# Kernel tuning notes

Hardware: AMD Instinct MI355X
Metric: run time of the kernel (lower is better)

The kernel has to match this reference:

```python
import jax, jax.numpy as jnp
import numpy as np

IN_FEAT = 3 * 299 * 299  # 268203
D1 = 512
H = 28
OUT = 2


def setup_inputs() -> dict:
    key = jax.random.key(0)
    ks = jax.random.split(key, 10)
    B, T = 4, 64
    s1 = 1.0 / np.sqrt(IN_FEAT)
    s2 = 1.0 / np.sqrt(D1)
    s3 = 1.0 / np.sqrt(H)
    return {
        "x": jax.random.normal(ks[0], (B, T, 3, 299, 299), jnp.float32),
        "W1": jax.random.uniform(ks[1], (IN_FEAT, D1), jnp.float32, -s1, s1),
        "b1": jax.random.uniform(ks[2], (D1,), jnp.float32, -s1, s1),
        "Wi": jax.random.uniform(ks[3], (D1, H), jnp.float32, -s2, s2),
        "Wr": jax.random.uniform(ks[4], (H, H), jnp.float32, -s3, s3),
        "br": jax.random.uniform(ks[5], (H,), jnp.float32, -s3, s3),
        "A": jax.random.normal(ks[6], (H,), jnp.float32),
        "tau": 1.0 + jax.random.uniform(ks[7], (H,), jnp.float32),  # positive time constants
        "W2": jax.random.uniform(ks[8], (H, OUT), jnp.float32, -s3, s3),
        "b2": jax.random.uniform(ks[9], (OUT,), jnp.float32, -s3, s3),
    }


def reference(x, W1, b1, Wi, Wr, br, A, tau, W2, b2):
    B, T = x.shape[0], x.shape[1]
    xf = x.reshape(B, T, -1)                      # [B, T, 268203]
    h1 = jax.nn.relu(jnp.einsum('btf,fd->btd', xf, W1) + b1)  # [B, T, 512]
    u = jnp.einsum('btd,dh->bth', h1, Wi)         # precomputed input drive [B, T, H]
    dt = 1.0

    def step(h, u_t):
        # fused-Euler LTC cell: f gates both time-constant and attractor A
        ft = jax.nn.sigmoid(u_t + h @ Wr + br)
        h_new = (h + dt * ft * A) / (1.0 + dt * (1.0 / tau + ft))
        return h_new, h_new

    h0 = jnp.zeros((B, H), x.dtype)
    _, hs = jax.lax.scan(step, h0, jnp.swapaxes(u, 0, 1))  # [T, B, H]
    last = jax.nn.relu(hs[-1])                    # relu then take last step
    out = last @ W2 + b2                          # [B, 2]
    return jax.nn.sigmoid(out)
```

## Files before the change

### kernel.cpp

```cpp
#include <hip/hip_runtime.h>
#include <hip/hip_bf16.h>

#define KTOT   268203
#define MROWS  256
#define NCOLS  512
#define HDIM   28
#define NSTEPS 8382
#define FSTEP  8381
#define KREM   11
#define BN     256
#define BROWS  40

typedef __attribute__((ext_vector_type(4))) float        f32x4;
typedef __attribute__((ext_vector_type(4))) unsigned int u32x4;
typedef __attribute__((ext_vector_type(8))) __bf16       bf16x8;

static __device__ inline bf16x8 pack8(const float* f) {
    union { bf16x8 v; __hip_bfloat16 h[8]; } u;
    #pragma unroll
    for (int j = 0; j < 8; ++j) u.h[j] = __float2bfloat16(f[j]);
    return u.v;
}
static __device__ inline unsigned short bfbits(float v) {
    __hip_bfloat16 h = __float2bfloat16(v);
    union { __hip_bfloat16 h; unsigned short u; } c; c.h = h; return c.u;
}

__global__ __launch_bounds__(512, 2) void gemm1_kernel(
    const float* __restrict__ x, const float* __restrict__ W1,
    __hip_bfloat16* __restrict__ part, int steps_per, int nks)
{
    __shared__ __align__(16) float          Albuf[2][MROWS * 32];
    __shared__ __align__(16) __hip_bfloat16 Blds[2][BN * BROWS];

    const int tid  = threadIdx.x;
    const int lane = tid & 63;
    const int w    = tid >> 6;
    const int wm   = w >> 1;
    const int wn   = w & 1;

    int bx, ks;
    {
        const int id = blockIdx.x;
        if ((nks & 7) == 0) {
            const int xcd = id & 7;
            const int m_  = id >> 3;
            bx = m_ & 1;
            ks = ((m_ >> 1) << 3) | xcd;
        } else {
            bx = id & 1;
            ks = id >> 1;
        }
    }
    const int bcol = bx * BN;

    const int dlt = lane >> 5;
    const int m   = lane & 31;
    const int rw7 = (2 * w + dlt) & 7;
    const int ag  = (m >> 2) ^ rw7;
    const size_t a_off = (size_t)(2 * w + dlt) * KTOT + ag * 4 + (m & 3);
    const int bkh  = w >> 2;
    const int bcl  = (w & 3) * 64 + lane;

    f32x4 acc[4][8];
    #pragma unroll
    for (int i = 0; i < 4; ++i)
        #pragma unroll
        for (int j = 0; j < 8; ++j)
            acc[i][j] = (f32x4){0.f, 0.f, 0.f, 0.f};

    const int s0 = ks * steps_per;
    int s1 = s0 + steps_per;
    if (s1 > NSTEPS) s1 = NSTEPS;
    int s1f = (s1 < FSTEP) ? s1 : FSTEP;
    int nfull = s1f - s0;
    if (nfull < 0) nfull = 0;

    float bregA[16], bregB[16];

    auto issueA = [&](int s, int buf) {
        const float* ap = x + a_off + (size_t)s * 32;
        #pragma unroll
        for (int i = 0; i < 16; ++i) {
            const float* gp = ap + (size_t)i * 16 * KTOT;
            char* lp = (char*)&Albuf[buf][0] + (i * 8 + w) * 256;
            __builtin_amdgcn_global_load_lds(
                (const __attribute__((address_space(1))) unsigned int*)(const void*)gp,
                (__attribute__((address_space(3))) unsigned int*)(void*)lp, 4, 0, 0);
        }
    };
    auto loadB = [&](int s, float* breg) {
        const float* bp = W1 + ((size_t)s * 32 + bkh * 16) * NCOLS + bcol + bcl;
        #pragma unroll
        for (int kk = 0; kk < 16; ++kk)
            breg[kk] = bp[(size_t)kk * NCOLS];
    };
    auto writeB = [&](const float* breg, int buf) {
        unsigned int pk[8];
        #pragma unroll
        for (int q = 0; q < 8; ++q)
            pk[q] = (unsigned int)bfbits(breg[2 * q]) |
                    ((unsigned int)bfbits(breg[2 * q + 1]) << 16);
        __hip_bfloat16* dst = &Blds[buf][bcl * BROWS + bkh * 16];
        *(u32x4*)(dst)     = (u32x4){pk[0], pk[1], pk[2], pk[3]};
        *(u32x4*)(dst + 8) = (u32x4){pk[4], pk[5], pk[6], pk[7]};
    };

    auto compute = [&](int buf) {
        const int rc = lane & 15, ko = lane >> 4;
        bf16x8 bq[8];
        #pragma unroll
        for (int ni = 0; ni < 8; ++ni)
            bq[ni] = *(const bf16x8*)&Blds[buf][(wn * 128 + ni * 16 + rc) * BROWS + ko * 8];
        const int soff = ((2 * ko) ^ (rc & 7)) * 16;
        #pragma unroll
        for (int mi = 0; mi < 4; ++mi) {
            const int ab = (wm * 64 + mi * 16 + rc) * 128;
            float afv[8];
            *(f32x4*)&afv[0] = *(const f32x4*)((const char*)&Albuf[buf][0] + ab + soff);
            *(f32x4*)&afv[4] = *(const f32x4*)((const char*)&Albuf[buf][0] + ab + (soff ^ 16));
            const bf16x8 af = pack8(afv);
            #pragma unroll
            for (int ni = 0; ni < 8; ++ni)
                acc[mi][ni] = __builtin_amdgcn_mfma_f32_16x16x32_bf16(
                    af, bq[ni], acc[mi][ni], 0, 0, 0);
        }
    };

    if (nfull > 0) {
        issueA(s0, 0); loadB(s0, bregA);
        if (nfull > 1) { issueA(s0 + 1, 1); loadB(s0 + 1, bregB); }
        int t = 0;
        for (;;) {
            if (t + 1 < nfull) { asm volatile("s_waitcnt vmcnt(32)" ::: "memory"); }
            else               { asm volatile("s_waitcnt vmcnt(0)"  ::: "memory"); }
            __builtin_amdgcn_sched_barrier(0);
            writeB(bregA, 0);
            asm volatile("s_waitcnt lgkmcnt(0)" ::: "memory");
            __builtin_amdgcn_sched_barrier(0);
            __builtin_amdgcn_s_barrier();
            __builtin_amdgcn_sched_barrier(0);
            compute(0);
            __builtin_amdgcn_sched_barrier(0);
            __builtin_amdgcn_s_barrier();
            if (t + 2 < nfull) { issueA(s0 + t + 2, 0); loadB(s0 + t + 2, bregA); }
            if (++t >= nfull) break;
            if (t + 1 < nfull) { asm volatile("s_waitcnt vmcnt(32)" ::: "memory"); }
            else               { asm volatile("s_waitcnt vmcnt(0)"  ::: "memory"); }
            __builtin_amdgcn_sched_barrier(0);
            writeB(bregB, 1);
            asm volatile("s_waitcnt lgkmcnt(0)" ::: "memory");
            __builtin_amdgcn_sched_barrier(0);
            __builtin_amdgcn_s_barrier();
            __builtin_amdgcn_sched_barrier(0);
            compute(1);
            __builtin_amdgcn_sched_barrier(0);
            __builtin_amdgcn_s_barrier();
            if (t + 2 < nfull) { issueA(s0 + t + 2, 1); loadB(s0 + t + 2, bregB); }
            if (++t >= nfull) break;
        }
    }

    if (s1 > FSTEP && s0 < s1) {
        const int buf = nfull & 1;
        __syncthreads();
        {
            const int row = tid >> 1, half = tid & 1;
            #pragma unroll
            for (int i = 0; i < 16; ++i) {
                const int k = half * 16 + i;
                const float v = (k < KREM)
                    ? x[(size_t)row * KTOT + (size_t)FSTEP * 32 + k] : 0.f;
                Albuf[buf][row * 32 + ((k >> 2) ^ (row & 7)) * 4 + (k & 3)] = v;
            }
        }
        {
            const int c = tid & 255, og = tid >> 8;
            #pragma unroll
            for (int i = 0; i < 16; ++i) {
                const int k = og * 16 + i;
                const float v = (k < KREM)
                    ? W1[(size_t)(FSTEP * 32 + k) * NCOLS + bcol + c] : 0.f;
                Blds[buf][c * BROWS + k] = __float2bfloat16(v);
            }
        }
        __syncthreads();
        compute(buf);
    }

    __hip_bfloat16* outp = part + (size_t)ks * MROWS * NCOLS;
    const int rc = lane & 15, q = lane >> 4;
    #pragma unroll
    for (int mi = 0; mi < 4; ++mi) {
        #pragma unroll
        for (int ni = 0; ni < 8; ++ni) {
            const int col = bcol + wn * 128 + ni * 16 + rc;
            #pragma unroll
            for (int j = 0; j < 4; ++j) {
                const int row = wm * 64 + mi * 16 + q * 4 + j;
                const float v  = acc[mi][ni][j];
                const float vh = __shfl_xor(v, 1);
                if (!(rc & 1)) {
                    const unsigned int pk =
                        (unsigned int)bfbits(v) | ((unsigned int)bfbits(vh) << 16);
                    *(unsigned int*)(outp + (size_t)row * NCOLS + col) = pk;
                }
            }
        }
    }
}

__global__ __launch_bounds__(512) void reduce_u_kernel(
    const __hip_bfloat16* __restrict__ part, const float* __restrict__ b1,
    const float* __restrict__ Wi, float* __restrict__ u, int nks)
{
    __shared__ float h1[NCOLS];
    __shared__ f32x4 red[4][128];
    const int row = blockIdx.x;
    const int tid = threadIdx.x;
    const int c4  = tid & 127;
    const int kk  = tid >> 7;

    const unsigned short* pu = (const unsigned short*)part;
    f32x4 sum = (f32x4){0.f, 0.f, 0.f, 0.f};
    for (int k = kk; k < nks; k += 4) {
        const size_t base = ((size_t)k * MROWS + row) * NCOLS + c4 * 4;
        ushort4 pv = *(const ushort4*)&pu[base];
        union { unsigned int u; float f; } c0, c1, c2, c3;
        c0.u = (unsigned int)pv.x << 16; c1.u = (unsigned int)pv.y << 16;
        c2.u = (unsigned int)pv.z << 16; c3.u = (unsigned int)pv.w << 16;
        sum[0] += c0.f; sum[1] += c1.f; sum[2] += c2.f; sum[3] += c3.f;
    }
    red[kk][c4] = sum;
    __syncthreads();

    if (tid < 128) {
        f32x4 t = red[0][tid] + red[1][tid] + red[2][tid] + red[3][tid];
        const f32x4 bb = *(const f32x4*)&b1[tid * 4];
        t += bb;
        #pragma unroll
        for (int j = 0; j < 4; ++j) h1[tid * 4 + j] = fmaxf(t[j], 0.f);
    }
    __syncthreads();

    const int wv = tid >> 6, lane = tid & 63;
    #pragma unroll
    for (int hh = 0; hh < 4; ++hh) {
        const int h = wv * 4 + hh;
        if (h < HDIM) {
            float p = 0.f;
            #pragma unroll
            for (int dd = 0; dd < 8; ++dd) {
                const int d = lane + dd * 64;
                p += h1[d] * Wi[d * HDIM + h];
            }
            #pragma unroll
            for (int off = 32; off; off >>= 1) p += __shfl_down(p, off);
            if (lane == 0) u[row * HDIM + h] = p;
        }
    }
}

__global__ __launch_bounds__(64) void recur_kernel(
    const float* __restrict__ u, const float* __restrict__ Wr,
    const float* __restrict__ br, const float* __restrict__ Av,
    const float* __restrict__ tau, const float* __restrict__ W2,
    const float* __restrict__ b2, float* __restrict__ out)
{
    const int b = blockIdx.x;
    const int j = threadIdx.x;
    const bool act = j < HDIM;
    const int jj = act ? j : 0;

    float wr[HDIM];
    #pragma unroll
    for (int i = 0; i < HDIM; ++i) wr[i] = act ? Wr[i * HDIM + jj] : 0.f;
    const float brj = act ? br[jj] : 0.f;
    const float Aj  = act ? Av[jj] : 0.f;
    const float itj = act ? (1.f / tau[jj]) : 0.f;

    float uv[64];
    #pragma unroll
    for (int t = 0; t < 64; ++t)
        uv[t] = act ? u[(b * 64 + t) * HDIM + jj] : 0.f;

    float h = 0.f;
    #pragma unroll
    for (int t = 0; t < 64; ++t) {
        float a = uv[t] + brj;
        #pragma unroll
        for (int i = 0; i < HDIM; ++i)
            a += __shfl(h, i) * wr[i];
        const float ft = 1.f / (1.f + expf(-a));
        const float hn = (h + ft * Aj) / (1.f + itj + ft);
        h = act ? hn : 0.f;
    }

    const float r  = act ? fmaxf(h, 0.f) : 0.f;
    float p0 = act ? r * W2[jj * 2 + 0] : 0.f;
    float p1 = act ? r * W2[jj * 2 + 1] : 0.f;
    #pragma unroll
    for (int off = 32; off; off >>= 1) {
        p0 += __shfl_down(p0, off);
        p1 += __shfl_down(p1, off);
    }
    if (j == 0) {
        out[b * 2 + 0] = 1.f / (1.f + expf(-(p0 + b2[0])));
        out[b * 2 + 1] = 1.f / (1.f + expf(-(p1 + b2[1])));
    }
}

extern "C" void kernel_launch(void* const* d_in, const int* in_sizes, int n_in,
                              void* d_out, int out_size, void* d_ws, size_t ws_size,
                              hipStream_t stream)
{
    (void)in_sizes; (void)n_in; (void)out_size;
    const float* x   = (const float*)d_in[0];
    const float* W1  = (const float*)d_in[1];
    const float* b1  = (const float*)d_in[2];
    const float* Wi  = (const float*)d_in[3];
    const float* Wr  = (const float*)d_in[4];
    const float* br  = (const float*)d_in[5];
    const float* Av  = (const float*)d_in[6];
    const float* tau = (const float*)d_in[7];
    const float* W2  = (const float*)d_in[8];
    const float* b2  = (const float*)d_in[9];
    float* out = (float*)d_out;

    const size_t per_split = (size_t)MROWS * NCOLS * sizeof(__hip_bfloat16);
    int nks = 128;
    while (nks > 8 && (size_t)nks * per_split + (1 << 16) > ws_size) nks >>= 1;
    const int steps_per = (NSTEPS + nks - 1) / nks;

    __hip_bfloat16* part = (__hip_bfloat16*)d_ws;
    float* u = (float*)((char*)d_ws + (size_t)nks * per_split);

    gemm1_kernel<<<dim3(2 * nks), 512, 0, stream>>>(x, W1, part, steps_per, nks);
    reduce_u_kernel<<<dim3(MROWS), 512, 0, stream>>>(part, b1, Wi, u, nks);
    recur_kernel<<<dim3(4), 64, 0, stream>>>(u, Wr, br, Av, tau, W2, b2, out);
}
```

Before: 270.3 us.

## Shrink GEMM1 column tile to 128 with 256-thread blocks and 4x grid

Halves the N tile of the split-K GEMM from 256 to 128 columns and the block from 8 to 4 waves, launching four column blocks per K-split instead of two. Each wave now covers 64 rows by all 128 columns, the B LDS tile drops its padding (stride 32 instead of 40), and each thread issues 32 direct-to-LDS A loads per step instead of 16. The aim is more blocks and smaller LDS per block for better occupancy and latency hiding. The cost is that the x tile, the dominant operand, is now read from global memory four times instead of twice, and the unpadded B layout may cause LDS bank conflicts.

```diff
diff --git a/kernel.cpp b/kernel.cpp
--- a/kernel.cpp
+++ b/kernel.cpp
@@ -8,8 +8,7 @@
 #define NSTEPS 8382
 #define FSTEP  8381
 #define KREM   11
-#define BN     256
-#define BROWS  40
+#define BN     128
 
 typedef __attribute__((ext_vector_type(4))) float        f32x4;
 typedef __attribute__((ext_vector_type(4))) unsigned int u32x4;
@@ -26,41 +25,40 @@
     union { __hip_bfloat16 h; unsigned short u; } c; c.h = h; return c.u;
 }
 
-__global__ __launch_bounds__(512, 2) void gemm1_kernel(
+__global__ __launch_bounds__(256, 2) void gemm1_kernel(
     const float* __restrict__ x, const float* __restrict__ W1,
     __hip_bfloat16* __restrict__ part, int steps_per, int nks)
 {
     __shared__ __align__(16) float          Albuf[2][MROWS * 32];
-    __shared__ __align__(16) __hip_bfloat16 Blds[2][BN * BROWS];
+    __shared__ __align__(16) __hip_bfloat16 Blds[2][BN * 32];
 
     const int tid  = threadIdx.x;
     const int lane = tid & 63;
     const int w    = tid >> 6;
-    const int wm   = w >> 1;
-    const int wn   = w & 1;
+    const int wm   = w;
 
     int bx, ks;
     {
         const int id = blockIdx.x;
         if ((nks & 7) == 0) {
-            const int xcd = id & 7;
-            const int m_  = id >> 3;
-            bx = m_ & 1;
-            ks = ((m_ >> 1) << 3) | xcd;
+            const int xcd  = id & 7;
+            const int rest = id >> 3;
+            bx = rest & 3;
+            ks = ((rest >> 2) << 3) | xcd;
         } else {
-            bx = id & 1;
-            ks = id >> 1;
+            bx = id & 3;
+            ks = id >> 2;
         }
     }
     const int bcol = bx * BN;
 
     const int dlt = lane >> 5;
     const int m   = lane & 31;
-    const int rw7 = (2 * w + dlt) & 7;
+    const int rw7 = 2 * w + dlt;
     const int ag  = (m >> 2) ^ rw7;
-    const size_t a_off = (size_t)(2 * w + dlt) * KTOT + ag * 4 + (m & 3);
-    const int bkh  = w >> 2;
-    const int bcl  = (w & 3) * 64 + lane;
+    const size_t a_off = (size_t)rw7 * KTOT + ag * 4 + (m & 3);
+    const int bcl = tid & 127;
+    const int bkh = tid >> 7;
 
     f32x4 acc[4][8];
     #pragma unroll
@@ -81,9 +79,9 @@
     auto issueA = [&](int s, int buf) {
         const float* ap = x + a_off + (size_t)s * 32;
         #pragma unroll
-        for (int i = 0; i < 16; ++i) {
-            const float* gp = ap + (size_t)i * 16 * KTOT;
-            char* lp = (char*)&Albuf[buf][0] + (i * 8 + w) * 256;
+        for (int i = 0; i < 32; ++i) {
+            const float* gp = ap + (size_t)i * 8 * KTOT;
+            char* lp = (char*)&Albuf[buf][0] + (i * 8 + 2 * w) * 128;
             __builtin_amdgcn_global_load_lds(
                 (const __attribute__((address_space(1))) unsigned int*)(const void*)gp,
                 (__attribute__((address_space(3))) unsigned int*)(void*)lp, 4, 0, 0);
@@ -101,7 +99,7 @@
         for (int q = 0; q < 8; ++q)
             pk[q] = (unsigned int)bfbits(breg[2 * q]) |
                     ((unsigned int)bfbits(breg[2 * q + 1]) << 16);
-        __hip_bfloat16* dst = &Blds[buf][bcl * BROWS + bkh * 16];
+        __hip_bfloat16* dst = &Blds[buf][bcl * 32 + bkh * 16];
         *(u32x4*)(dst)     = (u32x4){pk[0], pk[1], pk[2], pk[3]};
         *(u32x4*)(dst + 8) = (u32x4){pk[4], pk[5], pk[6], pk[7]};
     };
@@ -111,7 +109,7 @@
         bf16x8 bq[8];
         #pragma unroll
         for (int ni = 0; ni < 8; ++ni)
-            bq[ni] = *(const bf16x8*)&Blds[buf][(wn * 128 + ni * 16 + rc) * BROWS + ko * 8];
+            bq[ni] = *(const bf16x8*)&Blds[buf][(ni * 16 + rc) * 32 + ko * 8];
         const int soff = ((2 * ko) ^ (rc & 7)) * 16;
         #pragma unroll
         for (int mi = 0; mi < 4; ++mi) {
@@ -132,7 +130,7 @@
         if (nfull > 1) { issueA(s0 + 1, 1); loadB(s0 + 1, bregB); }
         int t = 0;
         for (;;) {
-            if (t + 1 < nfull) { asm volatile("s_waitcnt vmcnt(32)" ::: "memory"); }
+            if (t + 1 < nfull) { asm volatile("s_waitcnt vmcnt(48)" ::: "memory"); }
             else               { asm volatile("s_waitcnt vmcnt(0)"  ::: "memory"); }
             __builtin_amdgcn_sched_barrier(0);
             writeB(bregA, 0);
@@ -145,7 +143,7 @@
             __builtin_amdgcn_s_barrier();
             if (t + 2 < nfull) { issueA(s0 + t + 2, 0); loadB(s0 + t + 2, bregA); }
             if (++t >= nfull) break;
-            if (t + 1 < nfull) { asm volatile("s_waitcnt vmcnt(32)" ::: "memory"); }
+            if (t + 1 < nfull) { asm volatile("s_waitcnt vmcnt(48)" ::: "memory"); }
             else               { asm volatile("s_waitcnt vmcnt(0)"  ::: "memory"); }
             __builtin_amdgcn_sched_barrier(0);
             writeB(bregB, 1);
@@ -165,23 +163,21 @@
         const int buf = nfull & 1;
         __syncthreads();
         {
-            const int row = tid >> 1, half = tid & 1;
-            #pragma unroll
-            for (int i = 0; i < 16; ++i) {
-                const int k = half * 16 + i;
+            const int row = tid;
+            #pragma unroll
+            for (int k = 0; k < 32; ++k) {
                 const float v = (k < KREM)
                     ? x[(size_t)row * KTOT + (size_t)FSTEP * 32 + k] : 0.f;
                 Albuf[buf][row * 32 + ((k >> 2) ^ (row & 7)) * 4 + (k & 3)] = v;
             }
         }
         {
-            const int c = tid & 255, og = tid >> 8;
             #pragma unroll
             for (int i = 0; i < 16; ++i) {
-                const int k = og * 16 + i;
+                const int k = bkh * 16 + i;
                 const float v = (k < KREM)
-                    ? W1[(size_t)(FSTEP * 32 + k) * NCOLS + bcol + c] : 0.f;
-                Blds[buf][c * BROWS + k] = __float2bfloat16(v);
+                    ? W1[(size_t)(FSTEP * 32 + k) * NCOLS + bcol + bcl] : 0.f;
+                Blds[buf][bcl * 32 + k] = __float2bfloat16(v);
             }
         }
         __syncthreads();
@@ -194,7 +190,7 @@
     for (int mi = 0; mi < 4; ++mi) {
         #pragma unroll
         for (int ni = 0; ni < 8; ++ni) {
-            const int col = bcol + wn * 128 + ni * 16 + rc;
+            const int col = bcol + ni * 16 + rc;
             #pragma unroll
             for (int j = 0; j < 4; ++j) {
                 const int row = wm * 64 + mi * 16 + q * 4 + j;
@@ -335,7 +331,7 @@
     __hip_bfloat16* part = (__hip_bfloat16*)d_ws;
     float* u = (float*)((char*)d_ws + (size_t)nks * per_split);
 
-    gemm1_kernel<<<dim3(2 * nks), 512, 0, stream>>>(x, W1, part, steps_per, nks);
+    gemm1_kernel<<<dim3(4 * nks), 256, 0, stream>>>(x, W1, part, steps_per, nks);
     reduce_u_kernel<<<dim3(MROWS), 512, 0, stream>>>(part, b1, Wi, u, nks);
     recur_kernel<<<dim3(4), 64, 0, stream>>>(u, Wr, br, Av, tau, W2, b2, out);
 }
```

After: 271.0 us. No clear change (+0.3%).

## Triple-buffer LDS tiles to drop one barrier per k-step

Applied to the files above, without the earlier changes.

Moves from double to triple buffering of the A and B tiles in shared memory. The B register tile is written into the next buffer right after compute, and the next-next loads are issued at the same point. This removes the second workgroup barrier per iteration and keeps a single register set for B. It raises LDS use by about 50%, which could reduce occupancy below two blocks per CU. It also reorders the vmcnt accounting and makes the tail buffer index nfull%3.

```diff
diff --git a/kernel.cpp b/kernel.cpp
--- a/kernel.cpp
+++ b/kernel.cpp
@@ -30,8 +30,8 @@
     const float* __restrict__ x, const float* __restrict__ W1,
     __hip_bfloat16* __restrict__ part, int steps_per, int nks)
 {
-    __shared__ __align__(16) float          Albuf[2][MROWS * 32];
-    __shared__ __align__(16) __hip_bfloat16 Blds[2][BN * BROWS];
+    __shared__ __align__(16) float          Albuf[3][MROWS * 32];
+    __shared__ __align__(16) __hip_bfloat16 Blds[3][BN * BROWS];
 
     const int tid  = threadIdx.x;
     const int lane = tid & 63;
@@ -59,8 +59,8 @@
     const int rw7 = (2 * w + dlt) & 7;
     const int ag  = (m >> 2) ^ rw7;
     const size_t a_off = (size_t)(2 * w + dlt) * KTOT + ag * 4 + (m & 3);
-    const int bkh  = w >> 2;
-    const int bcl  = (w & 3) * 64 + lane;
+    const int bkh = w >> 2;
+    const int bcl = (w & 3) * 64 + lane;
 
     f32x4 acc[4][8];
     #pragma unroll
@@ -76,26 +76,27 @@
     int nfull = s1f - s0;
     if (nfull < 0) nfull = 0;
 
-    float bregA[16], bregB[16];
-
+    float breg[16];
+
+    auto loadB = [&](int s) {
+        const float* bp = W1 + ((size_t)s * 32 + bkh * 16) * NCOLS + bcol + bcl;
+        #pragma unroll
+        for (int kk = 0; kk < 16; ++kk)
+            breg[kk] = bp[(size_t)kk * NCOLS];
+    };
     auto issueA = [&](int s, int buf) {
         const float* ap = x + a_off + (size_t)s * 32;
+        float* lbase = &Albuf[buf][0];
         #pragma unroll
         for (int i = 0; i < 16; ++i) {
             const float* gp = ap + (size_t)i * 16 * KTOT;
-            char* lp = (char*)&Albuf[buf][0] + (i * 8 + w) * 256;
+            char* lp = (char*)lbase + (i * 8 + w) * 256;
             __builtin_amdgcn_global_load_lds(
                 (const __attribute__((address_space(1))) unsigned int*)(const void*)gp,
                 (__attribute__((address_space(3))) unsigned int*)(void*)lp, 4, 0, 0);
         }
     };
-    auto loadB = [&](int s, float* breg) {
-        const float* bp = W1 + ((size_t)s * 32 + bkh * 16) * NCOLS + bcol + bcl;
-        #pragma unroll
-        for (int kk = 0; kk < 16; ++kk)
-            breg[kk] = bp[(size_t)kk * NCOLS];
-    };
-    auto writeB = [&](const float* breg, int buf) {
+    auto writeB = [&](int buf) {
         unsigned int pk[8];
         #pragma unroll
         for (int q = 0; q < 8; ++q)
@@ -113,12 +114,13 @@
         for (int ni = 0; ni < 8; ++ni)
             bq[ni] = *(const bf16x8*)&Blds[buf][(wn * 128 + ni * 16 + rc) * BROWS + ko * 8];
         const int soff = ((2 * ko) ^ (rc & 7)) * 16;
+        const char* abase = (const char*)&Albuf[buf][0];
         #pragma unroll
         for (int mi = 0; mi < 4; ++mi) {
             const int ab = (wm * 64 + mi * 16 + rc) * 128;
             float afv[8];
-            *(f32x4*)&afv[0] = *(const f32x4*)((const char*)&Albuf[buf][0] + ab + soff);
-            *(f32x4*)&afv[4] = *(const f32x4*)((const char*)&Albuf[buf][0] + ab + (soff ^ 16));
+            *(f32x4*)&afv[0] = *(const f32x4*)(abase + ab + soff);
+            *(f32x4*)&afv[4] = *(const f32x4*)(abase + ab + (soff ^ 16));
             const bf16x8 af = pack8(afv);
             #pragma unroll
             for (int ni = 0; ni < 8; ++ni)
@@ -128,41 +130,41 @@
     };
 
     if (nfull > 0) {
-        issueA(s0, 0); loadB(s0, bregA);
-        if (nfull > 1) { issueA(s0 + 1, 1); loadB(s0 + 1, bregB); }
-        int t = 0;
-        for (;;) {
+        loadB(s0); issueA(s0, 0);
+        asm volatile("s_waitcnt vmcnt(16)" ::: "memory");
+        __builtin_amdgcn_sched_barrier(0);
+        writeB(0);
+        if (nfull > 1) { loadB(s0 + 1); issueA(s0 + 1, 1); }
+        asm volatile("s_waitcnt lgkmcnt(0)" ::: "memory");
+        __builtin_amdgcn_sched_barrier(0);
+
+        int buf = 0;
+        for (int t = 0; t < nfull; ++t) {
             if (t + 1 < nfull) { asm volatile("s_waitcnt vmcnt(32)" ::: "memory"); }
             else               { asm volatile("s_waitcnt vmcnt(0)"  ::: "memory"); }
             __builtin_amdgcn_sched_barrier(0);
-            writeB(bregA, 0);
-            asm volatile("s_waitcnt lgkmcnt(0)" ::: "memory");
-            __builtin_amdgcn_sched_barrier(0);
             __builtin_amdgcn_s_barrier();
             __builtin_amdgcn_sched_barrier(0);
-            compute(0);
+            compute(buf);
             __builtin_amdgcn_sched_barrier(0);
-            __builtin_amdgcn_s_barrier();
-            if (t + 2 < nfull) { issueA(s0 + t + 2, 0); loadB(s0 + t + 2, bregA); }
-            if (++t >= nfull) break;
-            if (t + 1 < nfull) { asm volatile("s_waitcnt vmcnt(32)" ::: "memory"); }
-            else               { asm volatile("s_waitcnt vmcnt(0)"  ::: "memory"); }
-            __builtin_amdgcn_sched_barrier(0);
-            writeB(bregB, 1);
-            asm volatile("s_waitcnt lgkmcnt(0)" ::: "memory");
-            __builtin_amdgcn_sched_barrier(0);
-            __builtin_amdgcn_s_barrier();
-            __builtin_amdgcn_sched_barrier(0);
-            compute(1);
-            __builtin_amdgcn_sched_barrier(0);
-            __builtin_amdgcn_s_barrier();
-            if (t + 2 < nfull) { issueA(s0 + t + 2, 1); loadB(s0 + t + 2, bregB); }
-            if (++t >= nfull) break;
+            if (t + 1 < nfull) {
+                asm volatile("s_waitcnt vmcnt(16)" ::: "memory");
+                __builtin_amdgcn_sched_barrier(0);
+                const int nb = (buf == 2) ? 0 : buf + 1;
+                writeB(nb);
+                if (t + 2 < nfull) {
+                    const int nnb = (nb == 2) ? 0 : nb + 1;
+                    loadB(s0 + t + 2); issueA(s0 + t + 2, nnb);
+                }
+                asm volatile("s_waitcnt lgkmcnt(0)" ::: "memory");
+                __builtin_amdgcn_sched_barrier(0);
+                buf = nb;
+            }
         }
     }
 
     if (s1 > FSTEP && s0 < s1) {
-        const int buf = nfull & 1;
+        const int buf = nfull % 3;
         __syncthreads();
         {
             const int row = tid >> 1, half = tid & 1;
```

After: 228.9 us, median of 3. 15.3% less time.
